# Kernel optimization log

Measured on AMD Instinct MI355X. Metric: run time of the kernel, lower is better.

Reference implementation:

```python
import jax, jax.numpy as jnp
import numpy as np

C = 64
EPS = 1e-5

def _layernorm(x, w, b):
    mu = jnp.mean(x, axis=-1, keepdims=True)
    var = jnp.var(x, axis=-1, keepdims=True)
    return (x - mu) * jax.lax.rsqrt(var + EPS) * w + b

def setup_inputs() -> dict:
    key = jax.random.key(0)
    ks = jax.random.split(key, 12)
    B, H, W = 4, 64, 64
    s = 1.0 / np.sqrt(C)
    inp = {
        'seg':   jax.random.normal(ks[0], (B, C, H, W), jnp.float32),
        'gauss': jax.random.normal(ks[1], (B, C, H, W), jnp.float32),
        'Wq': jax.random.normal(ks[2], (C, C), jnp.float32) * s,
        'bq': jnp.zeros((C,), jnp.float32),
        'Wk': jax.random.normal(ks[3], (C, C), jnp.float32) * s,
        'bk': jnp.zeros((C,), jnp.float32),
        'Wv': jax.random.normal(ks[4], (C, C), jnp.float32) * s,
        'bv': jnp.zeros((C,), jnp.float32),
        'ln1_w': jnp.ones((C,), jnp.float32),
        'ln1_b': jnp.zeros((C,), jnp.float32),
        'ln2_w': jnp.ones((C,), jnp.float32),
        'ln2_b': jnp.zeros((C,), jnp.float32),
        'W1': jax.random.normal(ks[5], (C, C), jnp.float32) * s,
        'b1': jnp.zeros((C,), jnp.float32),
        'W2': jax.random.normal(ks[6], (C, C), jnp.float32) * s,
        'b2': jnp.zeros((C,), jnp.float32),
    }
    return inp

def reference(seg, gauss, Wq, bq, Wk, bk, Wv, bv, ln1_w, ln1_b, ln2_w, ln2_b, W1, b1, W2, b2):
    B, Cc, H, W_ = seg.shape
    N = H * W_
    # 1x1 convs == per-pixel linear over channels; go straight to token layout
    seg_t = seg.reshape(B, Cc, N)      # [B,C,N]
    gau_t = gauss.reshape(B, Cc, N)
    q = jnp.einsum('bcn,oc->bno', seg_t, Wq) + bq        # [B,N,C]
    k = jnp.einsum('bcn,oc->bon', seg_t, Wk) + bk[None, :, None]  # [B,C,N]
    v = jnp.einsum('bcn,oc->bno', gau_t, Wv) + bv        # [B,N,C]
    scale = 1.0 / jnp.sqrt(jnp.float32(Cc))
    attn = jax.nn.softmax(jnp.einsum('bnc,bcm->bnm', q, k) * scale, axis=-1)  # [B,N,N]
    out = jnp.einsum('bnm,bmc->bnc', attn, v)
    x = _layernorm(v + out, ln1_w, ln1_b)
    ffn = jnp.einsum('bnc,oc->bno', jax.nn.relu(jnp.einsum('bnc,oc->bno', x, W1) + b1), W2) + b2
    x = _layernorm(x + ffn, ln2_w, ln2_b)
    return x.transpose(0, 2, 1).reshape(B, Cc, H, W_)
```

## Files before the change

kernel.cpp:

```cpp
#include <hip/hip_runtime.h>
#include <hip/hip_bf16.h>

typedef unsigned short u16;
typedef unsigned int u32;
typedef __attribute__((ext_vector_type(8))) short bf16x8;
typedef __attribute__((ext_vector_type(4))) float f32x4;

#define NTOK 4096
#define QSCALE2 0.18033688f

#define GLD_LDS(g, l) __builtin_amdgcn_global_load_lds( \
    (const __attribute__((address_space(1))) void*)(g), \
    (__attribute__((address_space(3))) void*)(l), 16, 0, 0)

__device__ __forceinline__ float b2f(u16 u) {
    u32 v = ((u32)u) << 16;
    return __builtin_bit_cast(float, v);
}
__device__ __forceinline__ u16 f2b(float f) {
    u32 u = __builtin_bit_cast(u32, f);
    u32 r = (u + 0x7fffu + ((u >> 16) & 1u)) >> 16;
    return (u16)r;
}
__device__ __forceinline__ u32 pack2(float lo, float hi) {
    return (u32)f2b(lo) | ((u32)f2b(hi) << 16);
}
__device__ __forceinline__ u32 pk2(float lo, float hi) {
    float2 t; t.x = lo; t.y = hi;
    __hip_bfloat162 b = __float22bfloat162_rn(t);
    u32 r;
    __builtin_memcpy(&r, &b, 4);
    return r;
}
__device__ __forceinline__ bf16x8 cvt8(const float* __restrict__ p) {
    float4 a = *(const float4*)p;
    float4 b = *(const float4*)(p + 4);
    bf16x8 r;
    r[0] = (short)f2b(a.x); r[1] = (short)f2b(a.y);
    r[2] = (short)f2b(a.z); r[3] = (short)f2b(a.w);
    r[4] = (short)f2b(b.x); r[5] = (short)f2b(b.y);
    r[6] = (short)f2b(b.z); r[7] = (short)f2b(b.w);
    return r;
}

__global__ __launch_bounds__(512) void qkv_kernel(
    const float* __restrict__ seg, const float* __restrict__ gau,
    const float* __restrict__ Wq, const float* __restrict__ bq,
    const float* __restrict__ Wk, const float* __restrict__ bk,
    const float* __restrict__ Wv, const float* __restrict__ bv,
    u16* __restrict__ Qt, u16* __restrict__ Kfrag,
    u16* __restrict__ Vtok, u16* __restrict__ Vswz)
{
    __shared__ __align__(16) u16 sSegT[64 * 64];
    __shared__ __align__(16) u16 sGauT[64 * 64];
    __shared__ __align__(16) u16 kBuf[64 * 64];
    const int tid = threadIdx.x;
    const int bid = blockIdx.x;
    const int xcd = bid & 7;
    const int b = xcd >> 1;
    const int nb = ((bid >> 3) << 1) | (xcd & 1);
    const int n0 = nb * 64;

    for (int idx = tid; idx < 4096; idx += 512) {
        int c = idx >> 6, t = idx & 63;
        int sw = t * 64 + ((((c >> 3) ^ (t & 7)) << 3) | (c & 7));
        sSegT[sw] = f2b(seg[(size_t)(b * 64 + c) * NTOK + n0 + t]);
        sGauT[sw] = f2b(gau[(size_t)(b * 64 + c) * NTOK + n0 + t]);
    }
    __syncthreads();

    const int lane = tid & 63;
    const int wv = tid >> 6;
    const int tb = wv & 3;
    const int task = wv >> 2;
    const int q = lane & 15, g = lane >> 4;
    const int tok = tb * 16 + q;

    const size_t obase = (size_t)b * NTOK * 64;
    const size_t rowb = (size_t)(n0 + tb * 16 + g * 4);

    if (task == 0) {
        bf16x8 as[2];
#pragma unroll
        for (int ks = 0; ks < 2; ++ks) {
            int c0 = ks * 32 + g * 8;
            int sw = tok * 64 + (((c0 >> 3) ^ (tok & 7)) << 3);
            as[ks] = *(const bf16x8*)&sSegT[sw];
        }
#pragma unroll
        for (int ob = 0; ob < 4; ++ob) {
            int o = ob * 16 + q;
            {
                float bias = bq[o];
                f32x4 acc = {bias, bias, bias, bias};
                bf16x8 w0 = cvt8(&Wq[o * 64 + g * 8]);
                bf16x8 w1 = cvt8(&Wq[o * 64 + 32 + g * 8]);
                acc = __builtin_amdgcn_mfma_f32_16x16x32_bf16(as[0], w0, acc, 0, 0, 0);
                acc = __builtin_amdgcn_mfma_f32_16x16x32_bf16(as[1], w1, acc, 0, 0, 0);
#pragma unroll
                for (int j = 0; j < 4; ++j)
                    Qt[obase + (rowb + j) * 64 + o] = f2b(acc[j] * QSCALE2);
            }
            {
                float bias = bk[o];
                f32x4 acc = {bias, bias, bias, bias};
                bf16x8 w0 = cvt8(&Wk[o * 64 + g * 8]);
                bf16x8 w1 = cvt8(&Wk[o * 64 + 32 + g * 8]);
                acc = __builtin_amdgcn_mfma_f32_16x16x32_bf16(as[0], w0, acc, 0, 0, 0);
                acc = __builtin_amdgcn_mfma_f32_16x16x32_bf16(as[1], w1, acc, 0, 0, 0);
#pragma unroll
                for (int j = 0; j < 4; ++j)
                    kBuf[(tb * 16 + g * 4 + j) * 64 + o] = f2b(acc[j]);
            }
        }
    } else {
        bf16x8 ag[2];
#pragma unroll
        for (int ks = 0; ks < 2; ++ks) {
            int c0 = ks * 32 + g * 8;
            int sw = tok * 64 + (((c0 >> 3) ^ (tok & 7)) << 3);
            ag[ks] = *(const bf16x8*)&sGauT[sw];
        }
        const int kbg = (n0 >> 5) + (tb >> 1);
        const int half = tb & 1;
#pragma unroll
        for (int ob = 0; ob < 4; ++ob) {
            int o = ob * 16 + q;
            float bias = bv[o];
            f32x4 acc = {bias, bias, bias, bias};
            bf16x8 w0 = cvt8(&Wv[o * 64 + g * 8]);
            bf16x8 w1 = cvt8(&Wv[o * 64 + 32 + g * 8]);
            acc = __builtin_amdgcn_mfma_f32_16x16x32_bf16(ag[0], w0, acc, 0, 0, 0);
            acc = __builtin_amdgcn_mfma_f32_16x16x32_bf16(ag[1], w1, acc, 0, 0, 0);
            ushort4 v4;
            v4.x = f2b(acc[0]); v4.y = f2b(acc[1]);
            v4.z = f2b(acc[2]); v4.w = f2b(acc[3]);
#pragma unroll
            for (int j = 0; j < 4; ++j)
                Vtok[obase + (rowb + j) * 64 + o] = f2b(acc[j]);
            *(ushort4*)&Vswz[(((size_t)(b * 128 + kbg)) * 4 + ob) * 512 + lane * 8 + half * 4] = v4;
        }
    }
    __syncthreads();

    {
        const int F = (wv * 64 + lane) * 8;
        const int kb2 = F >> 11;
        const int f = (F >> 9) & 3;
        const int l2 = (F >> 3) & 63;
        const int R = kb2 * 32 + ((f >> 1) << 4) + (l2 & 15);
        const int c0 = ((f & 1) << 5) + ((l2 >> 4) << 3);
        bf16x8 v = *(const bf16x8*)&kBuf[R * 64 + c0];
        *(bf16x8*)&Kfrag[(((size_t)(b * 128 + nb * 2 + kb2)) * 4 + f) * 512 + l2 * 8] = v;
    }
}

__global__ __launch_bounds__(512, 2) void attn_kernel(
    const u16* __restrict__ Qt, const u16* __restrict__ Kfrag,
    const u16* __restrict__ Vtok, const u16* __restrict__ Vswz,
    const float* __restrict__ ln1w, const float* __restrict__ ln1b,
    const float* __restrict__ ln2w, const float* __restrict__ ln2b,
    const float* __restrict__ W1, const float* __restrict__ b1,
    const float* __restrict__ W2, const float* __restrict__ b2,
    float* __restrict__ out)
{
    __shared__ __align__(16) u16 smem[8 * 2 * 4096];
    __shared__ __align__(16) u16 sX[2 * 16 * 64];
    __shared__ float sL[8][32];

    const int tid = threadIdx.x;
    const int wv = tid >> 6;
    const int lane = tid & 63;
    const int q = lane & 15, g = lane >> 4;
    const int bid = blockIdx.x;
    const int xcd = bid & 7;
    const int b = xcd >> 1;
    const int qb = ((bid >> 3) << 1) | (xcd & 1);
    const int q0 = qb * 32;
    const size_t tb_ = (size_t)b * NTOK * 64;

    const int n_qa = q0 + q, n_qb = q0 + 16 + q;
    bf16x8 qa0 = *(const bf16x8*)&Qt[tb_ + (size_t)n_qa * 64 + g * 8];
    bf16x8 qa1 = *(const bf16x8*)&Qt[tb_ + (size_t)n_qa * 64 + 32 + g * 8];
    bf16x8 qb0 = *(const bf16x8*)&Qt[tb_ + (size_t)n_qb * 64 + g * 8];
    bf16x8 qb1 = *(const bf16x8*)&Qt[tb_ + (size_t)n_qb * 64 + 32 + g * 8];

    f32x4 zero4 = {0.f, 0.f, 0.f, 0.f};
    f32x4 acc_a[4], acc_b[4];
#pragma unroll
    for (int i = 0; i < 4; ++i) { acc_a[i] = zero4; acc_b[i] = zero4; }
    float l_a = 0.f, l_b = 0.f;

    const int kbeg = wv * 512;
    const size_t kvb = ((size_t)(b * 128 + (kbeg >> 5))) * 2048;
    const u16* gK = Kfrag + kvb + lane * 8;
    const u16* gV = Vswz + kvb + lane * 8;
    u16* stW = &smem[wv * 8192];
    u16* lK = stW + lane * 8;

#pragma unroll
    for (int i = 0; i < 4; ++i) GLD_LDS(gK + i * 512, lK + i * 512);
#pragma unroll
    for (int i = 0; i < 4; ++i) GLD_LDS(gV + i * 512, lK + 2048 + i * 512);

    for (int it = 0; it < 16; ++it) {
        const int cur = it & 1;
        const u16* sb = &stW[cur * 4096];
        bf16x8 kf00 = *(const bf16x8*)&sb[0 * 512 + lane * 8];
        bf16x8 kf01 = *(const bf16x8*)&sb[1 * 512 + lane * 8];
        bf16x8 kf10 = *(const bf16x8*)&sb[2 * 512 + lane * 8];
        bf16x8 kf11 = *(const bf16x8*)&sb[3 * 512 + lane * 8];
        bf16x8 vf0 = *(const bf16x8*)&sb[2048 + 0 * 512 + lane * 8];
        bf16x8 vf1 = *(const bf16x8*)&sb[2048 + 1 * 512 + lane * 8];
        bf16x8 vf2 = *(const bf16x8*)&sb[2048 + 2 * 512 + lane * 8];
        bf16x8 vf3 = *(const bf16x8*)&sb[2048 + 3 * 512 + lane * 8];

        {
            const int tn = (it < 15) ? it + 1 : 15;
            const u16* gk = gK + (size_t)tn * 2048;
            const u16* gv = gV + (size_t)tn * 2048;
            u16* lk = lK + (cur ^ 1) * 4096;
#pragma unroll
            for (int i = 0; i < 4; ++i) GLD_LDS(gk + i * 512, lk + i * 512);
#pragma unroll
            for (int i = 0; i < 4; ++i) GLD_LDS(gv + i * 512, lk + 2048 + i * 512);
        }
        __builtin_amdgcn_sched_barrier(0);

        f32x4 s0a = __builtin_amdgcn_mfma_f32_16x16x32_bf16(kf00, qa0, zero4, 0, 0, 0);
        s0a = __builtin_amdgcn_mfma_f32_16x16x32_bf16(kf01, qa1, s0a, 0, 0, 0);
        f32x4 s1a = __builtin_amdgcn_mfma_f32_16x16x32_bf16(kf10, qa0, zero4, 0, 0, 0);
        s1a = __builtin_amdgcn_mfma_f32_16x16x32_bf16(kf11, qa1, s1a, 0, 0, 0);
        f32x4 s0b = __builtin_amdgcn_mfma_f32_16x16x32_bf16(kf00, qb0, zero4, 0, 0, 0);
        s0b = __builtin_amdgcn_mfma_f32_16x16x32_bf16(kf01, qb1, s0b, 0, 0, 0);
        f32x4 s1b = __builtin_amdgcn_mfma_f32_16x16x32_bf16(kf10, qb0, zero4, 0, 0, 0);
        s1b = __builtin_amdgcn_mfma_f32_16x16x32_bf16(kf11, qb1, s1b, 0, 0, 0);

        {
            float p0 = __builtin_exp2f(s0a[0]);
            float p1 = __builtin_exp2f(s0a[1]);
            float p2 = __builtin_exp2f(s0a[2]);
            float p3 = __builtin_exp2f(s0a[3]);
            float p4 = __builtin_exp2f(s1a[0]);
            float p5 = __builtin_exp2f(s1a[1]);
            float p6 = __builtin_exp2f(s1a[2]);
            float p7 = __builtin_exp2f(s1a[3]);
            l_a += ((p0 + p1) + (p2 + p3)) + ((p4 + p5) + (p6 + p7));
            u32 pwv[4] = {pk2(p0, p1), pk2(p2, p3), pk2(p4, p5), pk2(p6, p7)};
            bf16x8 pf = __builtin_bit_cast(bf16x8, *(const bf16x8*)pwv);
            acc_a[0] = __builtin_amdgcn_mfma_f32_16x16x32_bf16(vf0, pf, acc_a[0], 0, 0, 0);
            acc_a[1] = __builtin_amdgcn_mfma_f32_16x16x32_bf16(vf1, pf, acc_a[1], 0, 0, 0);
            acc_a[2] = __builtin_amdgcn_mfma_f32_16x16x32_bf16(vf2, pf, acc_a[2], 0, 0, 0);
            acc_a[3] = __builtin_amdgcn_mfma_f32_16x16x32_bf16(vf3, pf, acc_a[3], 0, 0, 0);
        }
        {
            float p0 = __builtin_exp2f(s0b[0]);
            float p1 = __builtin_exp2f(s0b[1]);
            float p2 = __builtin_exp2f(s0b[2]);
            float p3 = __builtin_exp2f(s0b[3]);
            float p4 = __builtin_exp2f(s1b[0]);
            float p5 = __builtin_exp2f(s1b[1]);
            float p6 = __builtin_exp2f(s1b[2]);
            float p7 = __builtin_exp2f(s1b[3]);
            l_b += ((p0 + p1) + (p2 + p3)) + ((p4 + p5) + (p6 + p7));
            u32 pwv[4] = {pk2(p0, p1), pk2(p2, p3), pk2(p4, p5), pk2(p6, p7)};
            bf16x8 pf = __builtin_bit_cast(bf16x8, *(const bf16x8*)pwv);
            acc_b[0] = __builtin_amdgcn_mfma_f32_16x16x32_bf16(vf0, pf, acc_b[0], 0, 0, 0);
            acc_b[1] = __builtin_amdgcn_mfma_f32_16x16x32_bf16(vf1, pf, acc_b[1], 0, 0, 0);
            acc_b[2] = __builtin_amdgcn_mfma_f32_16x16x32_bf16(vf2, pf, acc_b[2], 0, 0, 0);
            acc_b[3] = __builtin_amdgcn_mfma_f32_16x16x32_bf16(vf3, pf, acc_b[3], 0, 0, 0);
        }
    }

    l_a += __shfl_xor(l_a, 16); l_a += __shfl_xor(l_a, 32);
    l_b += __shfl_xor(l_b, 16); l_b += __shfl_xor(l_b, 32);

    asm volatile("s_waitcnt vmcnt(0)" ::: "memory");
    __syncthreads();
    float* sAcc = (float*)smem;
#define SACC(w_, r_) (&sAcc[(((w_) * 32) + (r_)) * 68])

    if (wv >= 4) {
        const int s = wv - 4;
        sL[wv][q] = l_a;      sL[wv][16 + q] = l_b;
#pragma unroll
        for (int cb = 0; cb < 4; ++cb) {
            *(f32x4*)&SACC(s, q)[cb * 16 + g * 4] = acc_a[cb];
            *(f32x4*)&SACC(s, 16 + q)[cb * 16 + g * 4] = acc_b[cb];
        }
    }
    __syncthreads();

    if (wv < 4) {
        l_a += sL[wv + 4][q];
        l_b += sL[wv + 4][16 + q];
#pragma unroll
        for (int cb = 0; cb < 4; ++cb) {
            f32x4 pa = *(const f32x4*)&SACC(wv, q)[cb * 16 + g * 4];
            f32x4 pb = *(const f32x4*)&SACC(wv, 16 + q)[cb * 16 + g * 4];
#pragma unroll
            for (int j = 0; j < 4; ++j) {
                acc_a[cb][j] += pa[j];
                acc_b[cb][j] += pb[j];
            }
        }
        sL[wv][q] = l_a;      sL[wv][16 + q] = l_b;
#pragma unroll
        for (int cb = 0; cb < 4; ++cb) {
            *(f32x4*)&SACC(wv, q)[cb * 16 + g * 4] = acc_a[cb];
            *(f32x4*)&SACC(wv, 16 + q)[cb * 16 + g * 4] = acc_b[cb];
        }
    }
    __syncthreads();
    if (wv >= 2) return;

    const int qe = wv * 16 + q;
    const int n_q = q0 + qe;

    float L = sL[0][qe] + sL[1][qe] + sL[2][qe] + sL[3][qe];
    f32x4 o[4];
#pragma unroll
    for (int cb = 0; cb < 4; ++cb) o[cb] = zero4;
#pragma unroll
    for (int w = 0; w < 4; ++w) {
#pragma unroll
        for (int cb = 0; cb < 4; ++cb) {
            f32x4 aw = *(const f32x4*)&SACC(w, qe)[cb * 16 + g * 4];
#pragma unroll
            for (int j = 0; j < 4; ++j) o[cb][j] += aw[j];
        }
    }

    float inv_l = 1.0f / L;
    float x1[4][4];
#pragma unroll
    for (int cb = 0; cb < 4; ++cb) {
        ushort4 vv = *(const ushort4*)&Vtok[tb_ + (size_t)n_q * 64 + cb * 16 + g * 4];
        x1[cb][0] = o[cb][0] * inv_l + b2f(vv.x);
        x1[cb][1] = o[cb][1] * inv_l + b2f(vv.y);
        x1[cb][2] = o[cb][2] * inv_l + b2f(vv.z);
        x1[cb][3] = o[cb][3] * inv_l + b2f(vv.w);
    }

    float s_ = 0.f;
#pragma unroll
    for (int cb = 0; cb < 4; ++cb)
        for (int j = 0; j < 4; ++j) s_ += x1[cb][j];
    s_ += __shfl_xor(s_, 16); s_ += __shfl_xor(s_, 32);
    float mean = s_ * (1.f / 64.f);
    float v_ = 0.f;
#pragma unroll
    for (int cb = 0; cb < 4; ++cb)
        for (int j = 0; j < 4; ++j) { float d = x1[cb][j] - mean; v_ += d * d; }
    v_ += __shfl_xor(v_, 16); v_ += __shfl_xor(v_, 32);
    float rstd = rsqrtf(v_ * (1.f / 64.f) + 1e-5f);

    float xh[4][4];
#pragma unroll
    for (int cb = 0; cb < 4; ++cb) {
        float4 lw = *(const float4*)&ln1w[cb * 16 + g * 4];
        float4 lb = *(const float4*)&ln1b[cb * 16 + g * 4];
        xh[cb][0] = (x1[cb][0] - mean) * rstd * lw.x + lb.x;
        xh[cb][1] = (x1[cb][1] - mean) * rstd * lw.y + lb.y;
        xh[cb][2] = (x1[cb][2] - mean) * rstd * lw.z + lb.z;
        xh[cb][3] = (x1[cb][3] - mean) * rstd * lw.w + lb.w;
    }

    u32* sXu = (u32*)sX;
    const int xwr = wv * 512 + q * 32;
#pragma unroll
    for (int cb = 0; cb < 4; ++cb) {
        sXu[xwr + cb * 8 + g * 2 + 0] = pack2(xh[cb][0], xh[cb][1]);
        sXu[xwr + cb * 8 + g * 2 + 1] = pack2(xh[cb][2], xh[cb][3]);
    }
    asm volatile("s_waitcnt lgkmcnt(0)" ::: "memory");
    __builtin_amdgcn_sched_barrier(0);
    const u16* xrp = &sX[wv * 1024 + q * 64 + g * 8];
    bf16x8 xb0 = *(const bf16x8*)&xrp[0];
    bf16x8 xb1 = *(const bf16x8*)&xrp[32];

    float h[4][4];
#pragma unroll
    for (int ob = 0; ob < 4; ++ob) {
        float4 bb = *(const float4*)&b1[ob * 16 + g * 4];
        f32x4 hacc = {bb.x, bb.y, bb.z, bb.w};
        bf16x8 w0 = cvt8(&W1[(size_t)(ob * 16 + q) * 64 + g * 8]);
        bf16x8 w1 = cvt8(&W1[(size_t)(ob * 16 + q) * 64 + 32 + g * 8]);
        hacc = __builtin_amdgcn_mfma_f32_16x16x32_bf16(w0, xb0, hacc, 0, 0, 0);
        hacc = __builtin_amdgcn_mfma_f32_16x16x32_bf16(w1, xb1, hacc, 0, 0, 0);
#pragma unroll
        for (int j = 0; j < 4; ++j) h[ob][j] = fmaxf(hacc[j], 0.f);
    }

#pragma unroll
    for (int ob = 0; ob < 4; ++ob) {
        sXu[xwr + ob * 8 + g * 2 + 0] = pack2(h[ob][0], h[ob][1]);
        sXu[xwr + ob * 8 + g * 2 + 1] = pack2(h[ob][2], h[ob][3]);
    }
    asm volatile("s_waitcnt lgkmcnt(0)" ::: "memory");
    __builtin_amdgcn_sched_barrier(0);
    bf16x8 hb0 = *(const bf16x8*)&xrp[0];
    bf16x8 hb1 = *(const bf16x8*)&xrp[32];

    float f_[4][4];
#pragma unroll
    for (int cb = 0; cb < 4; ++cb) {
        float4 bb = *(const float4*)&b2[cb * 16 + g * 4];
        f32x4 yacc = {bb.x, bb.y, bb.z, bb.w};
        bf16x8 w0 = cvt8(&W2[(size_t)(cb * 16 + q) * 64 + g * 8]);
        bf16x8 w1 = cvt8(&W2[(size_t)(cb * 16 + q) * 64 + 32 + g * 8]);
        yacc = __builtin_amdgcn_mfma_f32_16x16x32_bf16(w0, hb0, yacc, 0, 0, 0);
        yacc = __builtin_amdgcn_mfma_f32_16x16x32_bf16(w1, hb1, yacc, 0, 0, 0);
#pragma unroll
        for (int j = 0; j < 4; ++j) f_[cb][j] = xh[cb][j] + yacc[j];
    }

    float s2 = 0.f;
#pragma unroll
    for (int cb = 0; cb < 4; ++cb)
        for (int j = 0; j < 4; ++j) s2 += f_[cb][j];
    s2 += __shfl_xor(s2, 16); s2 += __shfl_xor(s2, 32);
    float mean2 = s2 * (1.f / 64.f);
    float v2 = 0.f;
#pragma unroll
    for (int cb = 0; cb < 4; ++cb)
        for (int j = 0; j < 4; ++j) { float d = f_[cb][j] - mean2; v2 += d * d; }
    v2 += __shfl_xor(v2, 16); v2 += __shfl_xor(v2, 32);
    float rstd2 = rsqrtf(v2 * (1.f / 64.f) + 1e-5f);

#pragma unroll
    for (int cb = 0; cb < 4; ++cb) {
        float4 lw = *(const float4*)&ln2w[cb * 16 + g * 4];
        float4 lb = *(const float4*)&ln2b[cb * 16 + g * 4];
        float o0 = (f_[cb][0] - mean2) * rstd2 * lw.x + lb.x;
        float o1 = (f_[cb][1] - mean2) * rstd2 * lw.y + lb.y;
        float o2 = (f_[cb][2] - mean2) * rstd2 * lw.z + lb.z;
        float o3 = (f_[cb][3] - mean2) * rstd2 * lw.w + lb.w;
        out[(size_t)(b * 64 + cb * 16 + g * 4 + 0) * NTOK + n_q] = o0;
        out[(size_t)(b * 64 + cb * 16 + g * 4 + 1) * NTOK + n_q] = o1;
        out[(size_t)(b * 64 + cb * 16 + g * 4 + 2) * NTOK + n_q] = o2;
        out[(size_t)(b * 64 + cb * 16 + g * 4 + 3) * NTOK + n_q] = o3;
    }
}

extern "C" void kernel_launch(void* const* d_in, const int* in_sizes, int n_in,
                              void* d_out, int out_size, void* d_ws, size_t ws_size,
                              hipStream_t stream) {
    const float* seg = (const float*)d_in[0];
    const float* gau = (const float*)d_in[1];
    const float* Wq = (const float*)d_in[2];
    const float* bq = (const float*)d_in[3];
    const float* Wk = (const float*)d_in[4];
    const float* bk = (const float*)d_in[5];
    const float* Wv = (const float*)d_in[6];
    const float* bv = (const float*)d_in[7];
    const float* ln1w = (const float*)d_in[8];
    const float* ln1b = (const float*)d_in[9];
    const float* ln2w = (const float*)d_in[10];
    const float* ln2b = (const float*)d_in[11];
    const float* W1 = (const float*)d_in[12];
    const float* b1 = (const float*)d_in[13];
    const float* W2 = (const float*)d_in[14];
    const float* b2 = (const float*)d_in[15];

    u16* Qt = (u16*)d_ws;
    u16* Kfrag = Qt + (size_t)4 * NTOK * 64;
    u16* Vtok = Kfrag + (size_t)4 * NTOK * 64;
    u16* Vswz = Vtok + (size_t)4 * NTOK * 64;
    float* outp = (float*)d_out;

    hipLaunchKernelGGL(qkv_kernel, dim3(256), dim3(512), 0, stream,
                       seg, gau, Wq, bq, Wk, bk, Wv, bv, Qt, Kfrag, Vtok, Vswz);
    hipLaunchKernelGGL(attn_kernel, dim3(512), dim3(512), 0, stream,
                       Qt, Kfrag, Vtok, Vswz, ln1w, ln1b, ln2w, ln2b,
                       W1, b1, W2, b2, outp);
}
```

Measured before the change: 59.58 us.

## Process 64 queries per block to reuse K/V tiles across four query groups

Each attention block now handles 64 query rows (four 16-row groups) instead of 32, halving the grid to 256 blocks. Each K/V fragment loaded into LDS is reused by twice as many MFMA query groups, which cuts global K/V traffic and LDS reads per unit of work. The cost is more accumulator registers per wave (16 f32x4 accumulators plus 8 Q fragments), which may lower occupancy under launch_bounds(512,2). The grid also shrinks to about one block per CU, reducing parallelism and latency hiding. The epilogue now uses four waves instead of two, and the sX and sL shared buffers are enlarged to match.

```diff
diff --git a/kernel.cpp b/kernel.cpp
--- a/kernel.cpp
+++ b/kernel.cpp
@@ -165,8 +165,8 @@
     float* __restrict__ out)
 {
     __shared__ __align__(16) u16 smem[8 * 2 * 4096];
-    __shared__ __align__(16) u16 sX[2 * 16 * 64];
-    __shared__ float sL[8][32];
+    __shared__ __align__(16) u16 sX[4 * 16 * 64];
+    __shared__ float sL[8][64];
 
     const int tid = threadIdx.x;
     const int wv = tid >> 6;
@@ -176,20 +176,24 @@
     const int xcd = bid & 7;
     const int b = xcd >> 1;
     const int qb = ((bid >> 3) << 1) | (xcd & 1);
-    const int q0 = qb * 32;
+    const int q0 = qb * 64;
     const size_t tb_ = (size_t)b * NTOK * 64;
 
-    const int n_qa = q0 + q, n_qb = q0 + 16 + q;
-    bf16x8 qa0 = *(const bf16x8*)&Qt[tb_ + (size_t)n_qa * 64 + g * 8];
-    bf16x8 qa1 = *(const bf16x8*)&Qt[tb_ + (size_t)n_qa * 64 + 32 + g * 8];
-    bf16x8 qb0 = *(const bf16x8*)&Qt[tb_ + (size_t)n_qb * 64 + g * 8];
-    bf16x8 qb1 = *(const bf16x8*)&Qt[tb_ + (size_t)n_qb * 64 + 32 + g * 8];
+    bf16x8 qf[4][2];
+#pragma unroll
+    for (int gi = 0; gi < 4; ++gi) {
+        const size_t r = tb_ + (size_t)(q0 + gi * 16 + q) * 64;
+        qf[gi][0] = *(const bf16x8*)&Qt[r + g * 8];
+        qf[gi][1] = *(const bf16x8*)&Qt[r + 32 + g * 8];
+    }
 
     f32x4 zero4 = {0.f, 0.f, 0.f, 0.f};
-    f32x4 acc_a[4], acc_b[4];
-#pragma unroll
-    for (int i = 0; i < 4; ++i) { acc_a[i] = zero4; acc_b[i] = zero4; }
-    float l_a = 0.f, l_b = 0.f;
+    f32x4 acc[4][4];
+#pragma unroll
+    for (int gi = 0; gi < 4; ++gi)
+#pragma unroll
+        for (int cb = 0; cb < 4; ++cb) acc[gi][cb] = zero4;
+    float l[4] = {0.f, 0.f, 0.f, 0.f};
 
     const int kbeg = wv * 512;
     const size_t kvb = ((size_t)(b * 128 + (kbeg >> 5))) * 2048;
@@ -227,92 +231,70 @@
         }
         __builtin_amdgcn_sched_barrier(0);
 
-        f32x4 s0a = __builtin_amdgcn_mfma_f32_16x16x32_bf16(kf00, qa0, zero4, 0, 0, 0);
-        s0a = __builtin_amdgcn_mfma_f32_16x16x32_bf16(kf01, qa1, s0a, 0, 0, 0);
-        f32x4 s1a = __builtin_amdgcn_mfma_f32_16x16x32_bf16(kf10, qa0, zero4, 0, 0, 0);
-        s1a = __builtin_amdgcn_mfma_f32_16x16x32_bf16(kf11, qa1, s1a, 0, 0, 0);
-        f32x4 s0b = __builtin_amdgcn_mfma_f32_16x16x32_bf16(kf00, qb0, zero4, 0, 0, 0);
-        s0b = __builtin_amdgcn_mfma_f32_16x16x32_bf16(kf01, qb1, s0b, 0, 0, 0);
-        f32x4 s1b = __builtin_amdgcn_mfma_f32_16x16x32_bf16(kf10, qb0, zero4, 0, 0, 0);
-        s1b = __builtin_amdgcn_mfma_f32_16x16x32_bf16(kf11, qb1, s1b, 0, 0, 0);
-
-        {
-            float p0 = __builtin_exp2f(s0a[0]);
-            float p1 = __builtin_exp2f(s0a[1]);
-            float p2 = __builtin_exp2f(s0a[2]);
-            float p3 = __builtin_exp2f(s0a[3]);
-            float p4 = __builtin_exp2f(s1a[0]);
-            float p5 = __builtin_exp2f(s1a[1]);
-            float p6 = __builtin_exp2f(s1a[2]);
-            float p7 = __builtin_exp2f(s1a[3]);
-            l_a += ((p0 + p1) + (p2 + p3)) + ((p4 + p5) + (p6 + p7));
+#pragma unroll
+        for (int gi = 0; gi < 4; ++gi) {
+            f32x4 s0 = __builtin_amdgcn_mfma_f32_16x16x32_bf16(kf00, qf[gi][0], zero4, 0, 0, 0);
+            s0 = __builtin_amdgcn_mfma_f32_16x16x32_bf16(kf01, qf[gi][1], s0, 0, 0, 0);
+            f32x4 s1 = __builtin_amdgcn_mfma_f32_16x16x32_bf16(kf10, qf[gi][0], zero4, 0, 0, 0);
+            s1 = __builtin_amdgcn_mfma_f32_16x16x32_bf16(kf11, qf[gi][1], s1, 0, 0, 0);
+
+            float p0 = __builtin_exp2f(s0[0]);
+            float p1 = __builtin_exp2f(s0[1]);
+            float p2 = __builtin_exp2f(s0[2]);
+            float p3 = __builtin_exp2f(s0[3]);
+            float p4 = __builtin_exp2f(s1[0]);
+            float p5 = __builtin_exp2f(s1[1]);
+            float p6 = __builtin_exp2f(s1[2]);
+            float p7 = __builtin_exp2f(s1[3]);
+            l[gi] += ((p0 + p1) + (p2 + p3)) + ((p4 + p5) + (p6 + p7));
             u32 pwv[4] = {pk2(p0, p1), pk2(p2, p3), pk2(p4, p5), pk2(p6, p7)};
             bf16x8 pf = __builtin_bit_cast(bf16x8, *(const bf16x8*)pwv);
-            acc_a[0] = __builtin_amdgcn_mfma_f32_16x16x32_bf16(vf0, pf, acc_a[0], 0, 0, 0);
-            acc_a[1] = __builtin_amdgcn_mfma_f32_16x16x32_bf16(vf1, pf, acc_a[1], 0, 0, 0);
-            acc_a[2] = __builtin_amdgcn_mfma_f32_16x16x32_bf16(vf2, pf, acc_a[2], 0, 0, 0);
-            acc_a[3] = __builtin_amdgcn_mfma_f32_16x16x32_bf16(vf3, pf, acc_a[3], 0, 0, 0);
-        }
-        {
-            float p0 = __builtin_exp2f(s0b[0]);
-            float p1 = __builtin_exp2f(s0b[1]);
-            float p2 = __builtin_exp2f(s0b[2]);
-            float p3 = __builtin_exp2f(s0b[3]);
-            float p4 = __builtin_exp2f(s1b[0]);
-            float p5 = __builtin_exp2f(s1b[1]);
-            float p6 = __builtin_exp2f(s1b[2]);
-            float p7 = __builtin_exp2f(s1b[3]);
-            l_b += ((p0 + p1) + (p2 + p3)) + ((p4 + p5) + (p6 + p7));
-            u32 pwv[4] = {pk2(p0, p1), pk2(p2, p3), pk2(p4, p5), pk2(p6, p7)};
-            bf16x8 pf = __builtin_bit_cast(bf16x8, *(const bf16x8*)pwv);
-            acc_b[0] = __builtin_amdgcn_mfma_f32_16x16x32_bf16(vf0, pf, acc_b[0], 0, 0, 0);
-            acc_b[1] = __builtin_amdgcn_mfma_f32_16x16x32_bf16(vf1, pf, acc_b[1], 0, 0, 0);
-            acc_b[2] = __builtin_amdgcn_mfma_f32_16x16x32_bf16(vf2, pf, acc_b[2], 0, 0, 0);
-            acc_b[3] = __builtin_amdgcn_mfma_f32_16x16x32_bf16(vf3, pf, acc_b[3], 0, 0, 0);
-        }
-    }
-
-    l_a += __shfl_xor(l_a, 16); l_a += __shfl_xor(l_a, 32);
-    l_b += __shfl_xor(l_b, 16); l_b += __shfl_xor(l_b, 32);
+            acc[gi][0] = __builtin_amdgcn_mfma_f32_16x16x32_bf16(vf0, pf, acc[gi][0], 0, 0, 0);
+            acc[gi][1] = __builtin_amdgcn_mfma_f32_16x16x32_bf16(vf1, pf, acc[gi][1], 0, 0, 0);
+            acc[gi][2] = __builtin_amdgcn_mfma_f32_16x16x32_bf16(vf2, pf, acc[gi][2], 0, 0, 0);
+            acc[gi][3] = __builtin_amdgcn_mfma_f32_16x16x32_bf16(vf3, pf, acc[gi][3], 0, 0, 0);
+        }
+    }
+
+#pragma unroll
+    for (int gi = 0; gi < 4; ++gi) {
+        l[gi] += __shfl_xor(l[gi], 16);
+        l[gi] += __shfl_xor(l[gi], 32);
+    }
 
     asm volatile("s_waitcnt vmcnt(0)" ::: "memory");
     __syncthreads();
     float* sAcc = (float*)smem;
-#define SACC(w_, r_) (&sAcc[(((w_) * 32) + (r_)) * 68])
+#define SACC(w_, r_) (&sAcc[(((w_) * 64) + (r_)) * 68])
 
     if (wv >= 4) {
         const int s = wv - 4;
-        sL[wv][q] = l_a;      sL[wv][16 + q] = l_b;
-#pragma unroll
-        for (int cb = 0; cb < 4; ++cb) {
-            *(f32x4*)&SACC(s, q)[cb * 16 + g * 4] = acc_a[cb];
-            *(f32x4*)&SACC(s, 16 + q)[cb * 16 + g * 4] = acc_b[cb];
+#pragma unroll
+        for (int gi = 0; gi < 4; ++gi) {
+            sL[wv][gi * 16 + q] = l[gi];
+#pragma unroll
+            for (int cb = 0; cb < 4; ++cb)
+                *(f32x4*)&SACC(s, gi * 16 + q)[cb * 16 + g * 4] = acc[gi][cb];
         }
     }
     __syncthreads();
 
     if (wv < 4) {
-        l_a += sL[wv + 4][q];
-        l_b += sL[wv + 4][16 + q];
-#pragma unroll
-        for (int cb = 0; cb < 4; ++cb) {
-            f32x4 pa = *(const f32x4*)&SACC(wv, q)[cb * 16 + g * 4];
-            f32x4 pb = *(const f32x4*)&SACC(wv, 16 + q)[cb * 16 + g * 4];
-#pragma unroll
-            for (int j = 0; j < 4; ++j) {
-                acc_a[cb][j] += pa[j];
-                acc_b[cb][j] += pb[j];
+#pragma unroll
+        for (int gi = 0; gi < 4; ++gi) {
+            l[gi] += sL[wv + 4][gi * 16 + q];
+            sL[wv][gi * 16 + q] = l[gi];
+#pragma unroll
+            for (int cb = 0; cb < 4; ++cb) {
+                f32x4 pa = *(const f32x4*)&SACC(wv, gi * 16 + q)[cb * 16 + g * 4];
+#pragma unroll
+                for (int j = 0; j < 4; ++j) acc[gi][cb][j] += pa[j];
+                *(f32x4*)&SACC(wv, gi * 16 + q)[cb * 16 + g * 4] = acc[gi][cb];
             }
         }
-        sL[wv][q] = l_a;      sL[wv][16 + q] = l_b;
-#pragma unroll
-        for (int cb = 0; cb < 4; ++cb) {
-            *(f32x4*)&SACC(wv, q)[cb * 16 + g * 4] = acc_a[cb];
-            *(f32x4*)&SACC(wv, 16 + q)[cb * 16 + g * 4] = acc_b[cb];
-        }
     }
     __syncthreads();
-    if (wv >= 2) return;
+    if (wv >= 4) return;
 
     const int qe = wv * 16 + q;
     const int n_q = q0 + qe;
@@ -471,7 +453,7 @@
 
     hipLaunchKernelGGL(qkv_kernel, dim3(256), dim3(512), 0, stream,
                        seg, gau, Wq, bq, Wk, bk, Wv, bv, Qt, Kfrag, Vtok, Vswz);
-    hipLaunchKernelGGL(attn_kernel, dim3(512), dim3(512), 0, stream,
+    hipLaunchKernelGGL(attn_kernel, dim3(256), dim3(512), 0, stream,
                        Qt, Kfrag, Vtok, Vswz, ln1w, ln1b, ln2w, ln2b,
                        W1, b1, W2, b2, outp);
 }
```

Result: faster. 52.19 us (-12.4%).
